# Kernel optimization log

Hardware: AMD Instinct MI355X
Metric: run time of the kernel (lower is better)

## Reference

```python
import jax, jax.numpy as jnp
import numpy as np


def _unfold3x3(x):
    # Matches torch F.unfold(kernel=(3,3), padding=1): output (B, C*9, H*W)
    # with feature layout (c, kh, kw) -- channel-major, kernel-position minor.
    B, C, H, W = x.shape
    xp = jnp.pad(x, ((0, 0), (0, 0), (1, 1), (1, 1)))
    patches = jnp.stack(
        [xp[:, :, i:i + H, j:j + W] for i in range(3) for j in range(3)],
        axis=2,
    )  # (B, C, 9, H, W)
    return patches.reshape(B, C * 9, H * W)


def setup_inputs() -> dict:
    key = jax.random.key(0)
    x = jax.random.normal(key, (4, 64, 64, 64), dtype=jnp.float32)
    return {"x": x}


def reference(x):
    B, C, H, W = x.shape
    HW = H * W
    xu = _unfold3x3(x)  # (B, C*9, HW)
    # torch F.normalize(dim=2): L2-normalize each (b, feature) row over spatial dim
    norm = jnp.maximum(jnp.linalg.norm(xu, axis=2, keepdims=True), 1e-12)
    xu = xu / norm
    # dense correlation over all positions: (B, HW, HW)
    R = jnp.einsum('bdn,bdm->bnm', xu, xu)
    _, idx = jax.lax.top_k(R, 3)  # idx: (B, HW, 3)
    # gather the top-3 neighbor patch columns; fixed k=3 loop (structural, not data dim)
    stacks = []
    for k in range(3):
        idx_k = idx[:, :, k][:, None, :]                    # (B, 1, HW)
        g = jnp.take_along_axis(xu, idx_k, axis=2)          # (B, C*9, HW)
        # torch: permute(0,2,1).reshape(B, HW, -1, C) -> (B, HW, 9, C)
        stacks.append(jnp.transpose(g, (0, 2, 1)).reshape(B, HW, 9, C))
    K = jnp.concatenate(stacks, axis=2)                     # (B, HW, 27, C)
    Q = jnp.transpose(x.reshape(B, C, HW), (0, 2, 1))       # (B, HW, C)
    scores = jnp.einsum('bnc,bnkc->bnk', Q, K) / jnp.sqrt(jnp.float32(C))
    w = jax.nn.softmax(scores, axis=2)                      # (B, HW, 27)
    return jnp.einsum('bnk,bnkc->bnc', w, K)                # (B, HW, C)
```

## Files before the change

### kernel.cpp

```cpp
#include <hip/hip_runtime.h>
#include <cstdint>

typedef short short8 __attribute__((ext_vector_type(8)));
typedef float f32x16 __attribute__((ext_vector_type(16)));

#define NB 4
#define NN 4096
#define ND 576
#define BIGI 0x7FFFFFFF
#define NSLICE 16

#define INVN_OFF 9437184
#define CANDV_OFF 9439488
#define CANDI_OFF 10225920

#define MFMA __builtin_amdgcn_mfma_f32_32x32x16_bf16

__device__ __forceinline__ unsigned short f2bf(float f) {
    unsigned u = __float_as_uint(f);
    u += 0x7FFFu + ((u >> 16) & 1u);
    return (unsigned short)(u >> 16);
}

__device__ __forceinline__ void gload_lds16(const void* g, void* l) {
    __builtin_amdgcn_global_load_lds(
        (const __attribute__((address_space(1))) void*)g,
        (__attribute__((address_space(3))) void*)l, 16, 0, 0);
}

__device__ __forceinline__ void insert_cmp(float v, int m,
    float& v0, int& i0, float& v1, int& i1, float& v2, int& i2) {
    bool beat2 = (v > v2) || (v == v2 && m < i2);
    if (beat2) {
        bool beat1 = (v > v1) || (v == v1 && m < i1);
        if (beat1) {
            v2 = v1; i2 = i1;
            bool beat0 = (v > v0) || (v == v0 && m < i0);
            if (beat0) { v1 = v0; i1 = i0; v0 = v; i0 = m; }
            else       { v1 = v;  i1 = m; }
        } else { v2 = v; i2 = m; }
    }
}

__global__ __launch_bounds__(64) void norm_kernel(const float* __restrict__ x,
                                                  float* __restrict__ ws) {
    const int bc = blockIdx.x;
    const int lane = threadIdx.x;
    const float* xp = x + ((size_t)bc << 12);
    float colsum = 0.f, v0 = 0.f, v63 = 0.f;
    for (int h = 0; h < 64; ++h) {
        const float val = xp[(h << 6) + lane];
        const float sq = val * val;
        colsum += sq;
        if (h == 0)  v0 = sq;
        if (h == 63) v63 = sq;
    }
    float total = colsum, row0 = v0, row63 = v63;
    #pragma unroll
    for (int o = 32; o > 0; o >>= 1) {
        total += __shfl_xor(total, o);
        row0  += __shfl_xor(row0, o);
        row63 += __shfl_xor(row63, o);
    }
    const float col0  = __shfl(colsum, 0);
    const float col63 = __shfl(colsum, 63);
    const float c00 = __shfl(v0, 0),  c0e = __shfl(v0, 63);
    const float ce0 = __shfl(v63, 0), cee = __shfl(v63, 63);
    if (lane < 9) {
        const int dh = lane / 3 - 1, dw = lane % 3 - 1;
        float S = total;
        if (dh == 1)  S -= row0;
        if (dh == -1) S -= row63;
        if (dw == 1)  S -= col0;
        if (dw == -1) S -= col63;
        if (dh == 1  && dw == 1)  S += c00;
        if (dh == 1  && dw == -1) S += c0e;
        if (dh == -1 && dw == 1)  S += ce0;
        if (dh == -1 && dw == -1) S += cee;
        float nrm = fmaxf(sqrtf(S), 1e-12f);
        ws[INVN_OFF + bc * 9 + lane] = 1.0f / nrm;
    }
}

__global__ __launch_bounds__(256) void mat_kernel(const float* __restrict__ x,
                                                  float* __restrict__ ws) {
    const int bi = blockIdx.x;
    const int b = bi / 576;
    const int rem = bi - b * 576;
    const int nt = rem / 18;
    const int kc = rem - nt * 18;
    unsigned short* AH = (unsigned short*)ws;
    unsigned short* AL = AH + 9437184;
    const float* invn = ws + INVN_OFF + b * 576;
    const int tid = threadIdx.x;
    #pragma unroll
    for (int hf2 = 0; hf2 < 2; ++hf2) {
        const int g = tid + hf2 * 256;
        const int row = g >> 2, cp = g & 3;
        const int c = cp ^ ((row >> 1) & 3);
        const int k0 = c * 8;
        const int n = nt * 128 + row;
        const int h = n >> 6, wc = n & 63;
        union { unsigned short us[8]; float4 f4; } uh, ul;
        #pragma unroll
        for (int j = 0; j < 8; ++j) {
            const int d = kc * 32 + k0 + j;
            const int ch = d / 9;
            const int p = d - ch * 9;
            const int r = h + p / 3 - 1, s2 = wc + p % 3 - 1;
            float val = 0.f;
            if ((unsigned)r < 64u && (unsigned)s2 < 64u)
                val = x[((size_t)(b * 64 + ch) << 12) + (r << 6) + s2];
            val *= invn[d];
            const unsigned short hb = f2bf(val);
            const float hfv = __uint_as_float(((unsigned)hb) << 16);
            const unsigned short lb = f2bf(val - hfv);
            uh.us[j] = hb; ul.us[j] = lb;
        }
        ((float4*)AH)[(size_t)bi * 512 + g] = uh.f4;
        ((float4*)AL)[(size_t)bi * 512 + g] = ul.f4;
    }
}

__device__ __forceinline__ short8 ldfrag(const short* p) {
    union { short8 s8; float4 f4; } u;
    u.f4 = *(const float4*)p;
    return u.s8;
}

__global__ void __launch_bounds__(512, 2) gram_kernel(float* ws) {
    __shared__ short sm[65536];
    const int bx = blockIdx.x;
    const int b = bx >> 8;
    const int t = bx & 255;
    const int x = t & 7, g = t >> 3;
    const int I = (x >> 1) * 4 + (g >> 3);
    const int J = (x & 1) * 8 + (g & 7);
    const int tid = threadIdx.x;
    const int w = tid >> 6, lane = tid & 63;
    const int wn = w >> 2, wm = w & 3;
    const int l31 = lane & 31, kh2 = lane >> 5;

    const unsigned short* AH = (const unsigned short*)ws;
    const unsigned short* AL = AH + 9437184;

    const unsigned short* gplane = (((w >> 1) & 1) == 0) ? AH : AL;
    const int gtile = (w < 4) ? (2 * I + (w & 1)) : (2 * J + (w & 1));
    const unsigned short* gbase = gplane + (size_t)((b * 32 + gtile) * 18) * 4096;
    const int ldsReg = w * 4096;

    int aoff[2][2];
    int boff[4][2];
    #pragma unroll
    for (int mi = 0; mi < 2; ++mi)
        #pragma unroll
        for (int h = 0; h < 2; ++h) {
            const int row = (wm & 1) * 64 + mi * 32 + l31;
            const int c = kh2 + 2 * h;
            aoff[mi][h] = (wm >> 1) * 4096 + row * 32 + (c ^ ((row >> 1) & 3)) * 8;
        }
    #pragma unroll
    for (int ni = 0; ni < 4; ++ni)
        #pragma unroll
        for (int h = 0; h < 2; ++h) {
            const int row = ni * 32 + l31;
            const int c = kh2 + 2 * h;
            boff[ni][h] = wn * 4096 + row * 32 + (c ^ ((row >> 1) & 3)) * 8;
        }

    f32x16 acc[2][4];
    #pragma unroll
    for (int mi = 0; mi < 2; ++mi)
        #pragma unroll
        for (int ni = 0; ni < 4; ++ni)
            #pragma unroll
            for (int e = 0; e < 16; ++e) acc[mi][ni][e] = 0.f;

    {
        const unsigned short* gs = gbase;
        short* dst = sm + ldsReg;
        #pragma unroll
        for (int i = 0; i < 8; ++i)
            gload_lds16(gs + i * 512 + lane * 8, dst + i * 512 + lane * 8);
    }

    for (int kc = 0; kc < 18; ++kc) {
        if (kc < 17) {
            const unsigned short* gs = gbase + (size_t)(kc + 1) * 4096;
            short* dst = sm + ((kc + 1) & 1) * 32768 + ldsReg;
            #pragma unroll
            for (int i = 0; i < 8; ++i)
                gload_lds16(gs + i * 512 + lane * 8, dst + i * 512 + lane * 8);
            asm volatile("s_waitcnt vmcnt(8)" ::: "memory");
        } else {
            asm volatile("s_waitcnt vmcnt(0)" ::: "memory");
        }
        asm volatile("s_barrier" ::: "memory");
        const short* base = sm + (kc & 1) * 32768;
        #pragma unroll
        for (int h = 0; h < 2; ++h) {
            short8 amh[2], aml[2];
            #pragma unroll
            for (int mi = 0; mi < 2; ++mi) {
                amh[mi] = ldfrag(base + 16384 + aoff[mi][h]);
                aml[mi] = ldfrag(base + 24576 + aoff[mi][h]);
            }
            #pragma unroll
            for (int ni = 0; ni < 4; ++ni) {
                const short8 bh = ldfrag(base + boff[ni][h]);
                const short8 bl = ldfrag(base + 8192 + boff[ni][h]);
                #pragma unroll
                for (int mi = 0; mi < 2; ++mi) {
                    acc[mi][ni] = MFMA(amh[mi], bh, acc[mi][ni], 0, 0, 0);
                    acc[mi][ni] = MFMA(amh[mi], bl, acc[mi][ni], 0, 0, 0);
                    acc[mi][ni] = MFMA(aml[mi], bh, acc[mi][ni], 0, 0, 0);
                }
            }
        }
        asm volatile("s_barrier" ::: "memory");
    }

    float t0v[4], t1v[4], t2v[4];
    int   t0i[4], t1i[4], t2i[4];
    #pragma unroll
    for (int i = 0; i < 4; ++i) {
        t0v[i] = t1v[i] = t2v[i] = -INFINITY;
        t0i[i] = t1i[i] = t2i[i] = BIGI;
    }
    const int mbase = J * 256 + wm * 64 + kh2 * 4;
    #pragma unroll
    for (int ni = 0; ni < 4; ++ni)
        #pragma unroll
        for (int mi = 0; mi < 2; ++mi)
            #pragma unroll
            for (int v = 0; v < 16; ++v) {
                const int m = mbase + mi * 32 + (v & 3) + 8 * (v >> 2);
                insert_cmp(acc[mi][ni][v], m,
                           t0v[ni], t0i[ni], t1v[ni], t1i[ni], t2v[ni], t2i[ni]);
            }

    #pragma unroll
    for (int ni = 0; ni < 4; ++ni) {
        const float pv0 = __shfl_xor(t0v[ni], 32);
        const float pv1 = __shfl_xor(t1v[ni], 32);
        const float pv2 = __shfl_xor(t2v[ni], 32);
        const int pi0 = __shfl_xor(t0i[ni], 32);
        const int pi1 = __shfl_xor(t1i[ni], 32);
        const int pi2 = __shfl_xor(t2i[ni], 32);
        insert_cmp(pv0, pi0, t0v[ni], t0i[ni], t1v[ni], t1i[ni], t2v[ni], t2i[ni]);
        insert_cmp(pv1, pi1, t0v[ni], t0i[ni], t1v[ni], t1i[ni], t2v[ni], t2i[ni]);
        insert_cmp(pv2, pi2, t0v[ni], t0i[ni], t1v[ni], t1i[ni], t2v[ni], t2i[ni]);
    }
    __syncthreads();
    float* cv = (float*)sm;
    int*   ci = (int*)sm + 3072;
    if (kh2 == 0) {
        #pragma unroll
        for (int ni = 0; ni < 4; ++ni) {
            const int base2 = ((w * 4 + ni) * 32 + l31) * 3;
            cv[base2] = t0v[ni]; cv[base2 + 1] = t1v[ni]; cv[base2 + 2] = t2v[ni];
            ci[base2] = t0i[ni]; ci[base2 + 1] = t1i[ni]; ci[base2 + 2] = t2i[ni];
        }
    }
    __syncthreads();
    if (tid < 256) {
        const int wnr = tid >> 7, rl = tid & 127;
        const int ni = rl >> 5, l = rl & 31;
        float v0 = -INFINITY, v1 = -INFINITY, v2 = -INFINITY;
        int i0 = BIGI, i1 = BIGI, i2 = BIGI;
        #pragma unroll
        for (int wm2 = 0; wm2 < 4; ++wm2) {
            const int base2 = (((wnr * 4 + wm2) * 4 + ni) * 32 + l) * 3;
            #pragma unroll
            for (int j = 0; j < 3; ++j)
                insert_cmp(cv[base2 + j], ci[base2 + j], v0, i0, v1, i1, v2, i2);
        }
        const int n_glob = (2 * I + wnr) * 128 + ni * 32 + l;
        const size_t o = ((size_t)(b * NSLICE + J) * NN + n_glob) * 3;
        ws[CANDV_OFF + o] = v0; ws[CANDV_OFF + o + 1] = v1; ws[CANDV_OFF + o + 2] = v2;
        unsigned short* wi = (unsigned short*)(ws + CANDI_OFF);
        wi[o] = (unsigned short)i0; wi[o + 1] = (unsigned short)i1; wi[o + 2] = (unsigned short)i2;
    }
}

__global__ __launch_bounds__(256) void attn_kernel(const float* __restrict__ x,
                                                   const float* __restrict__ ws,
                                                   float* __restrict__ out) {
    const int wid = threadIdx.x >> 6;
    const int lane = threadIdx.x & 63;
    const int gw = blockIdx.x * 4 + wid;
    const int b = gw >> 12;
    const int n = gw & 4095;

    float v0 = -INFINITY, v1 = -INFINITY, v2 = -INFINITY;
    int i0 = BIGI, i1 = BIGI, i2 = BIGI;
    const unsigned short* wi = (const unsigned short*)(ws + CANDI_OFF);
    for (int s = 0; s < NSLICE; ++s) {
        const size_t o = ((size_t)(b * NSLICE + s) * NN + n) * 3;
        #pragma unroll
        for (int j = 0; j < 3; ++j)
            insert_cmp(ws[CANDV_OFF + o + j], (int)wi[o + j], v0, i0, v1, i1, v2, i2);
    }
    const int idx3[3] = {i0, i1, i2};

    int cc[9], dhh[9], dww[9];
    float inr[9];
    #pragma unroll
    for (int a = 0; a < 9; ++a) {
        const int d = a * 64 + lane;
        const int c = d / 9;
        const int p = d - c * 9;
        cc[a] = c; dhh[a] = p / 3 - 1; dww[a] = p - (p / 3) * 3 - 1;
        inr[a] = ws[INVN_OFF + b * ND + d];
    }
    const float q = x[((size_t)(b * 64 + lane) << 12) + n];

    float rv[27], sc[27];
    #pragma unroll
    for (int k = 0; k < 3; ++k) {
        const int m = idx3[k];
        const int hm = m >> 6, wm = m & 63;
        #pragma unroll
        for (int a = 0; a < 9; ++a) {
            const int r = hm + dhh[a], s2 = wm + dww[a];
            float val = 0.f;
            if ((unsigned)r < 64u && (unsigned)s2 < 64u)
                val = x[((size_t)(b * 64 + cc[a]) << 12) + (r << 6) + s2];
            const float rr = val * inr[a];
            rv[k * 9 + a] = rr;
            float t = q * rr;
            #pragma unroll
            for (int o2 = 32; o2 > 0; o2 >>= 1) t += __shfl_xor(t, o2);
            sc[k * 9 + a] = t * 0.125f;
        }
    }
    float mx = -INFINITY;
    #pragma unroll
    for (int u = 0; u < 27; ++u) mx = fmaxf(mx, sc[u]);
    float sum = 0.f;
    #pragma unroll
    for (int u = 0; u < 27; ++u) { const float e = expf(sc[u] - mx); sc[u] = e; sum += e; }
    const float inv = 1.0f / sum;
    float o = 0.f;
    #pragma unroll
    for (int u = 0; u < 27; ++u) o += sc[u] * rv[u];
    out[((size_t)gw << 6) + lane] = o * inv;
}

extern "C" void kernel_launch(void* const* d_in, const int* in_sizes, int n_in,
                              void* d_out, int out_size, void* d_ws, size_t ws_size,
                              hipStream_t stream) {
    (void)in_sizes; (void)n_in; (void)out_size; (void)ws_size;
    const float* x = (const float*)d_in[0];
    float* ws = (float*)d_ws;
    float* out = (float*)d_out;

    hipLaunchKernelGGL(norm_kernel, dim3(NB * 64), dim3(64), 0, stream, x, ws);
    hipLaunchKernelGGL(mat_kernel, dim3(2304), dim3(256), 0, stream, x, ws);
    hipLaunchKernelGGL(gram_kernel, dim3(1024), dim3(512), 0, stream, ws);
    hipLaunchKernelGGL(attn_kernel, dim3(4096), dim3(256), 0, stream, x, ws, out);
}
```

Before: 811.6 us.

## Load gram MFMA fragments directly from global memory instead of LDS staging

```diff
diff --git a/kernel.cpp b/kernel.cpp
--- a/kernel.cpp
+++ b/kernel.cpp
@@ -20,12 +20,6 @@
     unsigned u = __float_as_uint(f);
     u += 0x7FFFu + ((u >> 16) & 1u);
     return (unsigned short)(u >> 16);
-}
-
-__device__ __forceinline__ void gload_lds16(const void* g, void* l) {
-    __builtin_amdgcn_global_load_lds(
-        (const __attribute__((address_space(1))) void*)g,
-        (__attribute__((address_space(3))) void*)l, 16, 0, 0);
 }
 
 __device__ __forceinline__ void insert_cmp(float v, int m,
@@ -122,50 +116,57 @@
     }
 }
 
-__device__ __forceinline__ short8 ldfrag(const short* p) {
+__device__ __forceinline__ short8 ldfragG(const unsigned short* p) {
     union { short8 s8; float4 f4; } u;
     u.f4 = *(const float4*)p;
     return u.s8;
 }
 
-__global__ void __launch_bounds__(512, 2) gram_kernel(float* ws) {
-    __shared__ short sm[65536];
+__global__ void __launch_bounds__(256, 2) gram_kernel(float* ws) {
+    __shared__ float cv[1536];
+    __shared__ int   ci[1536];
     const int bx = blockIdx.x;
-    const int b = bx >> 8;
+    const int r = bx >> 8;
     const int t = bx & 255;
     const int x = t & 7, g = t >> 3;
-    const int I = (x >> 1) * 4 + (g >> 3);
-    const int J = (x & 1) * 8 + (g & 7);
+    const int b = r >> 1;
+    const int half = r & 1;
+    const int nt = 16 * half + 4 * (x >> 1) + (g >> 3);
+    const int ms = 8 * (x & 1) + (g & 7);
     const int tid = threadIdx.x;
     const int w = tid >> 6, lane = tid & 63;
-    const int wn = w >> 2, wm = w & 3;
     const int l31 = lane & 31, kh2 = lane >> 5;
 
     const unsigned short* AH = (const unsigned short*)ws;
     const unsigned short* AL = AH + 9437184;
 
-    const unsigned short* gplane = (((w >> 1) & 1) == 0) ? AH : AL;
-    const int gtile = (w < 4) ? (2 * I + (w & 1)) : (2 * J + (w & 1));
-    const unsigned short* gbase = gplane + (size_t)((b * 32 + gtile) * 18) * 4096;
-    const int ldsReg = w * 4096;
-
-    int aoff[2][2];
-    int boff[4][2];
-    #pragma unroll
-    for (int mi = 0; mi < 2; ++mi)
-        #pragma unroll
-        for (int h = 0; h < 2; ++h) {
-            const int row = (wm & 1) * 64 + mi * 32 + l31;
-            const int c = kh2 + 2 * h;
-            aoff[mi][h] = (wm >> 1) * 4096 + row * 32 + (c ^ ((row >> 1) & 3)) * 8;
-        }
+    const unsigned short* gAn[2] = {
+        AH + (size_t)((b * 32 + nt) * 18) * 4096,
+        AL + (size_t)((b * 32 + nt) * 18) * 4096 };
+    const unsigned short* gAm[2][2];
+    #pragma unroll
+    for (int mi = 0; mi < 2; ++mi) {
+        const int tile = 2 * ms + ((2 * w + mi) >> 2);
+        gAm[mi][0] = AH + (size_t)((b * 32 + tile) * 18) * 4096;
+        gAm[mi][1] = AL + (size_t)((b * 32 + tile) * 18) * 4096;
+    }
+
+    int boff[4][2], aoff[2][2];
     #pragma unroll
     for (int ni = 0; ni < 4; ++ni)
         #pragma unroll
         for (int h = 0; h < 2; ++h) {
             const int row = ni * 32 + l31;
             const int c = kh2 + 2 * h;
-            boff[ni][h] = wn * 4096 + row * 32 + (c ^ ((row >> 1) & 3)) * 8;
+            boff[ni][h] = row * 32 + (c ^ ((row >> 1) & 3)) * 8;
+        }
+    #pragma unroll
+    for (int mi = 0; mi < 2; ++mi)
+        #pragma unroll
+        for (int h = 0; h < 2; ++h) {
+            const int row = (w * 64 + mi * 32 + l31) & 127;
+            const int c = kh2 + 2 * h;
+            aoff[mi][h] = row * 32 + (c ^ ((row >> 1) & 3)) * 8;
         }
 
     f32x16 acc[2][4];
@@ -176,48 +177,30 @@
             #pragma unroll
             for (int e = 0; e < 16; ++e) acc[mi][ni][e] = 0.f;
 
-    {
-        const unsigned short* gs = gbase;
-        short* dst = sm + ldsReg;
-        #pragma unroll
-        for (int i = 0; i < 8; ++i)
-            gload_lds16(gs + i * 512 + lane * 8, dst + i * 512 + lane * 8);
-    }
-
     for (int kc = 0; kc < 18; ++kc) {
-        if (kc < 17) {
-            const unsigned short* gs = gbase + (size_t)(kc + 1) * 4096;
-            short* dst = sm + ((kc + 1) & 1) * 32768 + ldsReg;
-            #pragma unroll
-            for (int i = 0; i < 8; ++i)
-                gload_lds16(gs + i * 512 + lane * 8, dst + i * 512 + lane * 8);
-            asm volatile("s_waitcnt vmcnt(8)" ::: "memory");
-        } else {
-            asm volatile("s_waitcnt vmcnt(0)" ::: "memory");
-        }
-        asm volatile("s_barrier" ::: "memory");
-        const short* base = sm + (kc & 1) * 32768;
+        const int kb = kc * 4096;
         #pragma unroll
         for (int h = 0; h < 2; ++h) {
-            short8 amh[2], aml[2];
+            short8 amh[2], aml[2], bh[4], bl[4];
             #pragma unroll
             for (int mi = 0; mi < 2; ++mi) {
-                amh[mi] = ldfrag(base + 16384 + aoff[mi][h]);
-                aml[mi] = ldfrag(base + 24576 + aoff[mi][h]);
+                amh[mi] = ldfragG(gAm[mi][0] + kb + aoff[mi][h]);
+                aml[mi] = ldfragG(gAm[mi][1] + kb + aoff[mi][h]);
             }
             #pragma unroll
             for (int ni = 0; ni < 4; ++ni) {
-                const short8 bh = ldfrag(base + boff[ni][h]);
-                const short8 bl = ldfrag(base + 8192 + boff[ni][h]);
+                bh[ni] = ldfragG(gAn[0] + kb + boff[ni][h]);
+                bl[ni] = ldfragG(gAn[1] + kb + boff[ni][h]);
+            }
+            #pragma unroll
+            for (int ni = 0; ni < 4; ++ni)
                 #pragma unroll
                 for (int mi = 0; mi < 2; ++mi) {
-                    acc[mi][ni] = MFMA(amh[mi], bh, acc[mi][ni], 0, 0, 0);
-                    acc[mi][ni] = MFMA(amh[mi], bl, acc[mi][ni], 0, 0, 0);
-                    acc[mi][ni] = MFMA(aml[mi], bh, acc[mi][ni], 0, 0, 0);
+                    acc[mi][ni] = MFMA(amh[mi], bh[ni], acc[mi][ni], 0, 0, 0);
+                    acc[mi][ni] = MFMA(amh[mi], bl[ni], acc[mi][ni], 0, 0, 0);
+                    acc[mi][ni] = MFMA(aml[mi], bh[ni], acc[mi][ni], 0, 0, 0);
                 }
-            }
-        }
-        asm volatile("s_barrier" ::: "memory");
+        }
     }
 
     float t0v[4], t1v[4], t2v[4];
@@ -227,7 +210,7 @@
         t0v[i] = t1v[i] = t2v[i] = -INFINITY;
         t0i[i] = t1i[i] = t2i[i] = BIGI;
     }
-    const int mbase = J * 256 + wm * 64 + kh2 * 4;
+    const int mbase = ms * 256 + w * 64 + kh2 * 4;
     #pragma unroll
     for (int ni = 0; ni < 4; ++ni)
         #pragma unroll
@@ -252,8 +235,6 @@
         insert_cmp(pv2, pi2, t0v[ni], t0i[ni], t1v[ni], t1i[ni], t2v[ni], t2i[ni]);
     }
     __syncthreads();
-    float* cv = (float*)sm;
-    int*   ci = (int*)sm + 3072;
     if (kh2 == 0) {
         #pragma unroll
         for (int ni = 0; ni < 4; ++ni) {
@@ -263,20 +244,19 @@
         }
     }
     __syncthreads();
-    if (tid < 256) {
-        const int wnr = tid >> 7, rl = tid & 127;
-        const int ni = rl >> 5, l = rl & 31;
+    if (tid < 128) {
+        const int ni = tid >> 5, l = tid & 31;
         float v0 = -INFINITY, v1 = -INFINITY, v2 = -INFINITY;
         int i0 = BIGI, i1 = BIGI, i2 = BIGI;
         #pragma unroll
-        for (int wm2 = 0; wm2 < 4; ++wm2) {
-            const int base2 = (((wnr * 4 + wm2) * 4 + ni) * 32 + l) * 3;
+        for (int w2 = 0; w2 < 4; ++w2) {
+            const int base2 = ((w2 * 4 + ni) * 32 + l) * 3;
             #pragma unroll
             for (int j = 0; j < 3; ++j)
                 insert_cmp(cv[base2 + j], ci[base2 + j], v0, i0, v1, i1, v2, i2);
         }
-        const int n_glob = (2 * I + wnr) * 128 + ni * 32 + l;
-        const size_t o = ((size_t)(b * NSLICE + J) * NN + n_glob) * 3;
+        const int n_glob = nt * 128 + ni * 32 + l;
+        const size_t o = ((size_t)(b * NSLICE + ms) * NN + n_glob) * 3;
         ws[CANDV_OFF + o] = v0; ws[CANDV_OFF + o + 1] = v1; ws[CANDV_OFF + o + 2] = v2;
         unsigned short* wi = (unsigned short*)(ws + CANDI_OFF);
         wi[o] = (unsigned short)i0; wi[o + 1] = (unsigned short)i1; wi[o + 2] = (unsigned short)i2;
@@ -357,6 +337,6 @@
 
     hipLaunchKernelGGL(norm_kernel, dim3(NB * 64), dim3(64), 0, stream, x, ws);
     hipLaunchKernelGGL(mat_kernel, dim3(2304), dim3(256), 0, stream, x, ws);
-    hipLaunchKernelGGL(gram_kernel, dim3(1024), dim3(512), 0, stream, ws);
+    hipLaunchKernelGGL(gram_kernel, dim3(2048), dim3(256), 0, stream, ws);
     hipLaunchKernelGGL(attn_kernel, dim3(4096), dim3(256), 0, stream, x, ws, out);
 }
```

New measurement: 808.3 us. About the same (-0.4%).
